# Kernel optimization log

Measured on AMD Instinct MI355X. Metric: run time of the kernel, lower is better.

The kernel has to match this reference:

```python
import jax, jax.numpy as jnp
import numpy as np

N = 20000      # nodes
E = 640000     # edges (avg degree 32)
F_X = 256      # node feature dim
F_E = 256      # edge feature dim
D = 2048       # hidden width
D_OUT = 512    # final Linear out_channels
EPS = 1e-5     # torch LayerNorm default eps


def _glorot_like(k, fan_in, fan_out):
    # torch nn.Linear default: U(-1/sqrt(fan_in), 1/sqrt(fan_in))
    lim = (1.0 / fan_in) ** 0.5
    return jax.random.uniform(k, (fan_in, fan_out), minval=-lim, maxval=lim, dtype=jnp.float32)


def setup_inputs() -> dict:
    key = jax.random.key(0)
    ks = jax.random.split(key, 8)
    return {
        "x": jax.random.normal(ks[0], (N, F_X), dtype=jnp.float32),
        "edge_index": jax.random.randint(ks[1], (2, E), 0, N),
        "edge_attr": jax.random.normal(ks[2], (E, F_E), dtype=jnp.float32),
        # u = (u, nb, eb) in the original; unused by this setup (no conv1d/GraphNorm)
        "u_counts": jnp.array([N], dtype=jnp.int32),
        "nb": jnp.zeros((N,), dtype=jnp.int32),
        "eb": jnp.zeros((E,), dtype=jnp.int32),
        # learned params per setup
        "W1": _glorot_like(ks[3], F_X + F_E, D), "b1": jnp.zeros((D,), jnp.float32),
        "W3": _glorot_like(ks[4], D, D),         "b3": jnp.zeros((D,), jnp.float32),
        "ln_g": jnp.ones((D,), jnp.float32),      "ln_b": jnp.zeros((D,), jnp.float32),
        "W6": _glorot_like(ks[5], D + F_X + F_E, D), "b6": jnp.zeros((D,), jnp.float32),
        "W8": _glorot_like(ks[6], D, D_OUT),      "b8": jnp.zeros((D_OUT,), jnp.float32),
    }


def reference(x, edge_index, edge_attr, u_counts, nb, eb,
              W1, b1, W3, b3, ln_g, ln_b, W6, b6, W8, b8):
    # scatter_mean(edge_attr, col, dim=0, dim_size=N)
    col = edge_index[1]
    seg_sum = jax.ops.segment_sum(edge_attr, col, num_segments=N)           # [N, F_E]
    cnt = jax.ops.segment_sum(jnp.ones((edge_attr.shape[0],), edge_attr.dtype),
                              col, num_segments=N)                           # [N]
    agg = seg_sum / jnp.maximum(cnt, 1.0)[:, None]                           # mean; 0 for empty slots

    h0 = jnp.concatenate([agg, x], axis=1)                                   # [N, F_E+F_X]
    # layer 1-2: Linear -> ReLU
    h2 = jax.nn.relu(h0 @ W1 + b1)                                           # [N, D]
    # layer 3-4: Linear -> ReLU
    h4 = jax.nn.relu(h2 @ W3 + b3)                                           # [N, D]
    # layer 5: LayerNorm (affine)
    mu = jnp.mean(h4, axis=-1, keepdims=True)
    var = jnp.var(h4, axis=-1, keepdims=True)
    h5 = (h4 - mu) * jax.lax.rsqrt(var + EPS) * ln_g + ln_b
    # layer 6-7: Linear over concat(h5, merge_in) -> ReLU  (skip connection)
    h7 = jax.nn.relu(jnp.concatenate([h5, h0], axis=1) @ W6 + b6)            # [N, D]
    # layer 8: Linear -> out[-1]
    return h7 @ W8 + b8                                                      # [N, D_OUT]
```

## Files before the change

kernel.cpp:

```cpp
#include <hip/hip_runtime.h>

typedef unsigned short ushort_t;
typedef __attribute__((ext_vector_type(4))) float f32x4;
typedef __attribute__((ext_vector_type(8))) __bf16 bf16x8;
typedef __attribute__((ext_vector_type(4))) __bf16 bf16x4;
typedef __attribute__((ext_vector_type(8))) unsigned short u16x8;
typedef __attribute__((ext_vector_type(4))) unsigned short u16x4;

__device__ __forceinline__ unsigned short f2bf(float f) {
  union { float f; unsigned int u; } v; v.f = f;
  unsigned int u = v.u;
  u += 0x7fffu + ((u >> 16) & 1u);
  return (unsigned short)(u >> 16);
}

__device__ __forceinline__ float bf2f(unsigned short h) {
  union { unsigned int u; float f; } v; v.u = ((unsigned int)h) << 16;
  return v.f;
}

__device__ __forceinline__ void gload16(ushort_t* lds, const ushort_t* g) {
  __builtin_amdgcn_global_load_lds(
      (const __attribute__((address_space(1))) unsigned int*)g,
      (__attribute__((address_space(3))) unsigned int*)lds, 16, 0, 0);
}

__global__ __launch_bounds__(256)
void transpose_w(const float* __restrict__ in, ushort_t* __restrict__ out, int R, int C) {
  __shared__ float tile[32][33];
  const int t = threadIdx.x;
  const int tx = t & 31, ty = t >> 5;
  const int r0 = blockIdx.x * 32, c0 = blockIdx.y * 32;
#pragma unroll
  for (int i = 0; i < 4; ++i)
    tile[ty + 8 * i][tx] = in[(size_t)(r0 + ty + 8 * i) * C + c0 + tx];
  __syncthreads();
#pragma unroll
  for (int i = 0; i < 4; ++i)
    out[(size_t)(c0 + ty + 8 * i) * R + r0 + tx] = f2bf(tile[tx][ty + 8 * i]);
}

__global__ __launch_bounds__(256)
void count_edges(const int* __restrict__ col, int* __restrict__ cnt, int E) {
  int i = blockIdx.x * 256 + threadIdx.x;
  if (i < E) atomicAdd(&cnt[col[i]], 1);
}

__global__ __launch_bounds__(1024)
void prefix_kernel(const int* __restrict__ cnt, int* __restrict__ start,
                   int* __restrict__ cursor, int N) {
  const int t = threadIdx.x;
  const int chunk = (N + 1023) >> 10;
  const int base = t * chunk;
  int s = 0;
  for (int j = 0; j < chunk; ++j) {
    int i = base + j;
    s += (i < N) ? cnt[i] : 0;
  }
  const int lane = t & 63, wv = t >> 6;
  int scan = s;
#pragma unroll
  for (int o = 1; o < 64; o <<= 1) {
    int up = __shfl_up(scan, o);
    if (lane >= o) scan += up;
  }
  __shared__ int wsum[16];
  if (lane == 63) wsum[wv] = scan;
  __syncthreads();
  if (t == 0) {
    int acc = 0;
#pragma unroll
    for (int i2 = 0; i2 < 16; ++i2) { int v = wsum[i2]; wsum[i2] = acc; acc += v; }
  }
  __syncthreads();
  int run = wsum[wv] + (scan - s);
  for (int j = 0; j < chunk; ++j) {
    int i = base + j;
    if (i < N) {
      start[i] = run; cursor[i] = run;
      run += cnt[i];
    }
  }
}

__global__ __launch_bounds__(256)
void fill_csr(const int* __restrict__ col, int* __restrict__ cursor,
              int* __restrict__ eids, int E) {
  int i = blockIdx.x * 256 + threadIdx.x;
  if (i < E) {
    int p = atomicAdd(&cursor[col[i]], 1);
    eids[p] = i;
  }
}

__global__ __launch_bounds__(256)
void gather_mean(const float* __restrict__ eattr, const int* __restrict__ start,
                 const int* __restrict__ deg, const int* __restrict__ eids,
                 const float* __restrict__ x, ushort_t* __restrict__ hcat, int N) {
  const int row = blockIdx.x;
  const int t = threadIdx.x;
  const int w = t >> 6, l = t & 63;
  const int s = start[row], d = deg[row];
  const float4* ea4 = (const float4*)eattr;
  float4 sum = make_float4(0.f, 0.f, 0.f, 0.f);
  for (int i = w; i < d; i += 4) {
    int e = eids[s + i];
    float4 v = ea4[(size_t)e * 64 + l];
    sum.x += v.x; sum.y += v.y; sum.z += v.z; sum.w += v.w;
  }
  __shared__ float4 part[4][64];
  part[w][l] = sum;
  __syncthreads();
  hcat[(size_t)row * 2560 + 2304 + t] = f2bf(x[(size_t)row * 256 + t]);
  if (w == 0) {
    float4 a = part[0][l], b = part[1][l], c = part[2][l], dd = part[3][l];
    const float inv = 1.f / fmaxf((float)d, 1.f);
    u16x4 o;
    o[0] = f2bf((a.x + b.x + c.x + dd.x) * inv);
    o[1] = f2bf((a.y + b.y + c.y + dd.y) * inv);
    o[2] = f2bf((a.z + b.z + c.z + dd.z) * inv);
    o[3] = f2bf((a.w + b.w + c.w + dd.w) * inv);
    *(u16x4*)(hcat + (size_t)row * 2560 + 2048 + l * 4) = o;
  }
}

__global__ __launch_bounds__(256)
void ln_kernel(ushort_t* __restrict__ hcat, const float* __restrict__ g,
               const float* __restrict__ b) {
  const int row = blockIdx.x;
  const int t = threadIdx.x;
  ushort_t* p = hcat + (size_t)row * 2560 + t * 8;
  u16x8 raw = *(const u16x8*)p;
  float vv[8];
#pragma unroll
  for (int j = 0; j < 8; ++j) vv[j] = bf2f(raw[j]);
  float s = 0.f, ss = 0.f;
#pragma unroll
  for (int j = 0; j < 8; ++j) { s += vv[j]; ss += vv[j] * vv[j]; }
#pragma unroll
  for (int o = 32; o > 0; o >>= 1) {
    s += __shfl_xor(s, o);
    ss += __shfl_xor(ss, o);
  }
  __shared__ float red[8];
  int w = t >> 6, l = t & 63;
  if (l == 0) { red[w] = s; red[4 + w] = ss; }
  __syncthreads();
  s = red[0] + red[1] + red[2] + red[3];
  ss = red[4] + red[5] + red[6] + red[7];
  const float mu = s * (1.f / 2048.f);
  const float var = ss * (1.f / 2048.f) - mu * mu;
  const float rs = rsqrtf(var + 1e-5f);
  float4 g0 = *(const float4*)(g + t * 8);
  float4 g1 = *(const float4*)(g + t * 8 + 4);
  float4 b0 = *(const float4*)(b + t * 8);
  float4 b1 = *(const float4*)(b + t * 8 + 4);
  float gg[8] = {g0.x, g0.y, g0.z, g0.w, g1.x, g1.y, g1.z, g1.w};
  float bb[8] = {b0.x, b0.y, b0.z, b0.w, b1.x, b1.y, b1.z, b1.w};
  u16x8 o8;
#pragma unroll
  for (int j = 0; j < 8; ++j) o8[j] = f2bf((vv[j] - mu) * rs * gg[j] + bb[j]);
  *(u16x8*)p = o8;
}


#define SBAR() do { __builtin_amdgcn_sched_barrier(0); \
                    __builtin_amdgcn_s_barrier(); \
                    __builtin_amdgcn_sched_barrier(0); } while (0)

template <int RELU, int OUTBF>
__global__ __launch_bounds__(512, 4)
void gemm128(const ushort_t* __restrict__ A, int lda,
             const ushort_t* __restrict__ Bt,
             const float* __restrict__ bias,
             void* __restrict__ Cout, int ldc, int M, int K) {
  __shared__ __align__(16) ushort_t smem[36864];
  char* sb = (char*)smem;
  const int t = threadIdx.x;

  const int nct = gridDim.x;
  const int nwg = nct * gridDim.y;
  const int flat = blockIdx.y * nct + blockIdx.x;
  const int xcd = flat & 7, loc = flat >> 3;
  const int q = nwg >> 3, r = nwg & 7;
  const int swz = (xcd < r ? xcd * (q + 1) : r * (q + 1) + (xcd - r) * q) + loc;
  const int row0 = (swz / nct) * 128;
  const int col0 = (swz % nct) * 256;

  const int wid = t >> 6, l = t & 63;
  const int wr = wid >> 2, wc = wid & 3;
  const int lr = l & 15, lk = l >> 4;

  const int srow = t >> 2;
  const int scol = ((t & 3) ^ ((t >> 2) & 3)) << 3;
  int ar = row0 + srow; if (ar > M - 1) ar = M - 1;
  const ushort_t* pa  = A + (size_t)ar * lda + scol;
  const ushort_t* pb0 = Bt + (size_t)(col0 + srow) * K + scol;
  const ushort_t* pb1 = pb0 + (size_t)128 * K;
  const int tb = t * 16;

  const int sx = ((lk ^ (lr & 3)) << 4);
  const int arow = (wr * 64 + lr) * 64 + sx;
  const int brow = 8192 + (wc * 64 + lr) * 64 + sx;

  f32x4 acc[4][4] = {};

  const int nk = K >> 5;

  {
    const int k1 = (nk > 1) ? 32 : 0;
    gload16((ushort_t*)(sb + 8192 + tb), pb0);
    gload16((ushort_t*)(sb + 16384 + tb), pb1);
    gload16((ushort_t*)(sb + 0 + tb), pa);
    gload16((ushort_t*)(sb + 24576 + 8192 + tb), pb0 + k1);
    gload16((ushort_t*)(sb + 24576 + 16384 + tb), pb1 + k1);
    gload16((ushort_t*)(sb + 24576 + 0 + tb), pa + k1);
  }
  asm volatile("s_waitcnt vmcnt(3)" ::: "memory");
  SBAR();

  int cO = 0, sO = 49152;
  for (int k = 0; k < nk; ++k) {
    const int kc2 = ((k + 2 < nk) ? k + 2 : nk - 1) << 5;

    bf16x8 a[4], b[4];
#pragma unroll
    for (int m = 0; m < 4; ++m)
      a[m] = *(const bf16x8*)(sb + cO + arow + m * 1024);
#pragma unroll
    for (int n = 0; n < 4; ++n)
      b[n] = *(const bf16x8*)(sb + cO + brow + n * 1024);
    gload16((ushort_t*)(sb + sO + 8192 + tb), pb0 + kc2);
    gload16((ushort_t*)(sb + sO + 16384 + tb), pb1 + kc2);
    gload16((ushort_t*)(sb + sO + 0 + tb), pa + kc2);

    __builtin_amdgcn_s_setprio(1);
#pragma unroll
    for (int m = 0; m < 4; ++m)
#pragma unroll
      for (int n = 0; n < 4; ++n)
        acc[m][n] = __builtin_amdgcn_mfma_f32_16x16x32_bf16(b[n], a[m], acc[m][n], 0, 0, 0);
    __builtin_amdgcn_s_setprio(0);

    asm volatile("s_waitcnt vmcnt(3)" ::: "memory");
    SBAR();

    cO = (cO == 49152) ? 0 : cO + 24576;
    sO = (sO == 49152) ? 0 : sO + 24576;
  }
  asm volatile("s_waitcnt vmcnt(0)" ::: "memory");

#pragma unroll
  for (int mi = 0; mi < 4; ++mi) {
    const int orow = row0 + wr * 64 + mi * 16 + lr;
    if (orow < M) {
#pragma unroll
      for (int nj = 0; nj < 4; ++nj) {
        const int cb = col0 + wc * 64 + nj * 16 + lk * 4;
        const float4 bv = *(const float4*)(bias + cb);
        f32x4 v = acc[mi][nj];
        float o0 = v[0] + bv.x, o1 = v[1] + bv.y, o2 = v[2] + bv.z, o3 = v[3] + bv.w;
        if (RELU) {
          o0 = fmaxf(o0, 0.f); o1 = fmaxf(o1, 0.f);
          o2 = fmaxf(o2, 0.f); o3 = fmaxf(o3, 0.f);
        }
        if (OUTBF) {
          bf16x4 o;
          o[0] = (__bf16)o0; o[1] = (__bf16)o1; o[2] = (__bf16)o2; o[3] = (__bf16)o3;
          *(bf16x4*)((ushort_t*)Cout + (size_t)orow * ldc + cb) = o;
        } else {
          float4 ov = make_float4(o0, o1, o2, o3);
          *(float4*)((float*)Cout + (size_t)orow * ldc + cb) = ov;
        }
      }
    }
  }
}

extern "C" void kernel_launch(void* const* d_in, const int* in_sizes, int n_in,
                              void* d_out, int out_size, void* d_ws, size_t ws_size,
                              hipStream_t stream) {
  (void)n_in; (void)out_size; (void)ws_size;
  const float* x     = (const float*)d_in[0];
  const int*   eidx  = (const int*)d_in[1];
  const float* eattr = (const float*)d_in[2];
  const float* W1 = (const float*)d_in[6];
  const float* b1 = (const float*)d_in[7];
  const float* W3 = (const float*)d_in[8];
  const float* b3 = (const float*)d_in[9];
  const float* lng = (const float*)d_in[10];
  const float* lnb = (const float*)d_in[11];
  const float* W6 = (const float*)d_in[12];
  const float* b6 = (const float*)d_in[13];
  const float* W8 = (const float*)d_in[14];
  const float* b8 = (const float*)d_in[15];

  const int N = in_sizes[0] / 256;
  const int E = in_sizes[2] / 256;
  const int* col = eidx + E;

  char* ws = (char*)d_ws;
  size_t off = 0;
  ushort_t* hcat = (ushort_t*)(ws + off);  off += (size_t)N * 2560 * 2;
  ushort_t* h2   = (ushort_t*)(ws + off);  off += (size_t)N * 2048 * 2;
  ushort_t* W1t = (ushort_t*)(ws + off);   off += (size_t)2048 * 512 * 2;
  ushort_t* W3t = (ushort_t*)(ws + off);   off += (size_t)2048 * 2048 * 2;
  ushort_t* W6t = (ushort_t*)(ws + off);   off += (size_t)2048 * 2560 * 2;
  ushort_t* W8t = (ushort_t*)(ws + off);   off += (size_t)512 * 2048 * 2;
  int* deg    = (int*)(ws + off);  off += (size_t)N * 4;
  int* startp = (int*)(ws + off);  off += (size_t)N * 4;
  int* cursor = (int*)(ws + off);  off += (size_t)N * 4;
  int* eids   = (int*)(ws + off);  off += (size_t)E * 4;

  hipMemsetAsync(deg, 0, (size_t)N * 4, stream);

  transpose_w<<<dim3(512 / 32, 2048 / 32), 256, 0, stream>>>(W1, W1t, 512, 2048);
  transpose_w<<<dim3(2048 / 32, 2048 / 32), 256, 0, stream>>>(W3, W3t, 2048, 2048);
  transpose_w<<<dim3(2560 / 32, 2048 / 32), 256, 0, stream>>>(W6, W6t, 2560, 2048);
  transpose_w<<<dim3(2048 / 32, 512 / 32), 256, 0, stream>>>(W8, W8t, 2048, 512);

  count_edges<<<(E + 255) / 256, 256, 0, stream>>>(col, deg, E);
  prefix_kernel<<<1, 1024, 0, stream>>>(deg, startp, cursor, N);
  fill_csr<<<(E + 255) / 256, 256, 0, stream>>>(col, cursor, eids, E);
  gather_mean<<<N, 256, 0, stream>>>(eattr, startp, deg, eids, x, hcat, N);

  const int Mt = (N + 127) / 128;
  gemm128<1, 1><<<dim3(8, Mt), 512, 0, stream>>>(hcat + 2048, 2560, W1t, b1, h2, 2048, N, 512);
  gemm128<1, 1><<<dim3(8, Mt), 512, 0, stream>>>(h2, 2048, W3t, b3, hcat, 2560, N, 2048);
  ln_kernel<<<N, 256, 0, stream>>>(hcat, lng, lnb);
  gemm128<1, 1><<<dim3(8, Mt), 512, 0, stream>>>(hcat, 2560, W6t, b6, h2, 2048, N, 2560);
  gemm128<0, 0><<<dim3(2, Mt), 512, 0, stream>>>(h2, 2048, W8t, b8, (float*)d_out, 512, N, 2048);
}
```

Before: 842.7 us.

## Fuse weight transposes with edge counting, unroll gather, reorder GEMM prefetch

Merges the four weight-transpose launches and the edge-count kernel into a single launch that dispatches on block id, which cuts launch overhead. The gather-mean loop now gives each wave a contiguous chunk of edges and unrolls by four so more independent loads are in flight. The GEMM main loop issues its global-to-LDS prefetches before the LDS fragment reads, which may hide more latency but changes the ordering between the waitcnt and the LDS reads.

```diff
diff --git a/kernel.cpp b/kernel.cpp
--- a/kernel.cpp
+++ b/kernel.cpp
@@ -26,11 +26,27 @@
 }
 
 __global__ __launch_bounds__(256)
-void transpose_w(const float* __restrict__ in, ushort_t* __restrict__ out, int R, int C) {
+void prep_kernel(const float* __restrict__ W1, const float* __restrict__ W3,
+                 const float* __restrict__ W6, const float* __restrict__ W8,
+                 ushort_t* __restrict__ W1t, ushort_t* __restrict__ W3t,
+                 ushort_t* __restrict__ W6t, ushort_t* __restrict__ W8t,
+                 const int* __restrict__ col, int* __restrict__ deg, int E) {
+  const int bid = blockIdx.x;
+  const int t = threadIdx.x;
+  if (bid >= 11264) {
+    int i = (bid - 11264) * 256 + t;
+    if (i < E) atomicAdd(&deg[col[i]], 1);
+    return;
+  }
+  const float* in; ushort_t* out; int R, C, lb;
+  if (bid < 1024)       { in = W1; out = W1t; R = 512;  C = 2048; lb = bid; }
+  else if (bid < 5120)  { in = W3; out = W3t; R = 2048; C = 2048; lb = bid - 1024; }
+  else if (bid < 10240) { in = W6; out = W6t; R = 2560; C = 2048; lb = bid - 5120; }
+  else                  { in = W8; out = W8t; R = 2048; C = 512;  lb = bid - 10240; }
   __shared__ float tile[32][33];
-  const int t = threadIdx.x;
   const int tx = t & 31, ty = t >> 5;
-  const int r0 = blockIdx.x * 32, c0 = blockIdx.y * 32;
+  const int nrt = R >> 5;
+  const int r0 = (lb % nrt) * 32, c0 = (lb / nrt) * 32;
 #pragma unroll
   for (int i = 0; i < 4; ++i)
     tile[ty + 8 * i][tx] = in[(size_t)(r0 + ty + 8 * i) * C + c0 + tx];
@@ -38,12 +54,6 @@
 #pragma unroll
   for (int i = 0; i < 4; ++i)
     out[(size_t)(c0 + ty + 8 * i) * R + r0 + tx] = f2bf(tile[tx][ty + 8 * i]);
-}
-
-__global__ __launch_bounds__(256)
-void count_edges(const int* __restrict__ col, int* __restrict__ cnt, int E) {
-  int i = blockIdx.x * 256 + threadIdx.x;
-  if (i < E) atomicAdd(&cnt[col[i]], 1);
 }
 
 __global__ __launch_bounds__(1024)
@@ -103,9 +113,23 @@
   const int s = start[row], d = deg[row];
   const float4* ea4 = (const float4*)eattr;
   float4 sum = make_float4(0.f, 0.f, 0.f, 0.f);
-  for (int i = w; i < d; i += 4) {
-    int e = eids[s + i];
-    float4 v = ea4[(size_t)e * 64 + l];
+  const int chunk = (d + 3) >> 2;
+  const int i0 = w * chunk;
+  const int i1 = (d < i0 + chunk) ? d : i0 + chunk;
+  int i = i0;
+  for (; i + 4 <= i1; i += 4) {
+    int e0 = eids[s + i], e1 = eids[s + i + 1], e2 = eids[s + i + 2], e3 = eids[s + i + 3];
+    float4 v0 = ea4[(size_t)e0 * 64 + l];
+    float4 v1 = ea4[(size_t)e1 * 64 + l];
+    float4 v2 = ea4[(size_t)e2 * 64 + l];
+    float4 v3 = ea4[(size_t)e3 * 64 + l];
+    sum.x += v0.x + v1.x + v2.x + v3.x;
+    sum.y += v0.y + v1.y + v2.y + v3.y;
+    sum.z += v0.z + v1.z + v2.z + v3.z;
+    sum.w += v0.w + v1.w + v2.w + v3.w;
+  }
+  for (; i < i1; ++i) {
+    float4 v = ea4[(size_t)eids[s + i] * 64 + l];
     sum.x += v.x; sum.y += v.y; sum.z += v.z; sum.w += v.w;
   }
   __shared__ float4 part[4][64];
@@ -204,7 +228,6 @@
   const int brow = 8192 + (wc * 64 + lr) * 64 + sx;
 
   f32x4 acc[4][4] = {};
-
   const int nk = K >> 5;
 
   {
@@ -223,16 +246,17 @@
   for (int k = 0; k < nk; ++k) {
     const int kc2 = ((k + 2 < nk) ? k + 2 : nk - 1) << 5;
 
-    bf16x8 a[4], b[4];
-#pragma unroll
-    for (int m = 0; m < 4; ++m)
-      a[m] = *(const bf16x8*)(sb + cO + arow + m * 1024);
-#pragma unroll
-    for (int n = 0; n < 4; ++n)
-      b[n] = *(const bf16x8*)(sb + cO + brow + n * 1024);
     gload16((ushort_t*)(sb + sO + 8192 + tb), pb0 + kc2);
     gload16((ushort_t*)(sb + sO + 16384 + tb), pb1 + kc2);
     gload16((ushort_t*)(sb + sO + 0 + tb), pa + kc2);
+
+    bf16x8 a[4], b[4];
+#pragma unroll
+    for (int m = 0; m < 4; ++m)
+      a[m] = *(const bf16x8*)(sb + cO + arow + m * 1024);
+#pragma unroll
+    for (int n = 0; n < 4; ++n)
+      b[n] = *(const bf16x8*)(sb + cO + brow + n * 1024);
 
     __builtin_amdgcn_s_setprio(1);
 #pragma unroll
@@ -314,14 +338,11 @@
 
   hipMemsetAsync(deg, 0, (size_t)N * 4, stream);
 
-  transpose_w<<<dim3(512 / 32, 2048 / 32), 256, 0, stream>>>(W1, W1t, 512, 2048);
-  transpose_w<<<dim3(2048 / 32, 2048 / 32), 256, 0, stream>>>(W3, W3t, 2048, 2048);
-  transpose_w<<<dim3(2560 / 32, 2048 / 32), 256, 0, stream>>>(W6, W6t, 2560, 2048);
-  transpose_w<<<dim3(2048 / 32, 512 / 32), 256, 0, stream>>>(W8, W8t, 2048, 512);
-
-  count_edges<<<(E + 255) / 256, 256, 0, stream>>>(col, deg, E);
+  const int cntBlocks = (E + 255) / 256;
+  prep_kernel<<<11264 + cntBlocks, 256, 0, stream>>>(W1, W3, W6, W8, W1t, W3t, W6t, W8t,
+                                                     col, deg, E);
   prefix_kernel<<<1, 1024, 0, stream>>>(deg, startp, cursor, N);
-  fill_csr<<<(E + 255) / 256, 256, 0, stream>>>(col, cursor, eids, E);
+  fill_csr<<<cntBlocks, 256, 0, stream>>>(col, cursor, eids, E);
   gather_mean<<<N, 256, 0, stream>>>(eattr, startp, deg, eids, x, hcat, N);
 
   const int Mt = (N + 127) / 128;
```

New measurement: 822.9 us. -2.4%, faster.
